# Performance work log

Hardware: AMD Instinct MI355X
Metric: run time of the kernel (lower is better)

## Reference

```python
import jax, jax.numpy as jnp
import numpy as np

INPUT_SIZE = 512
N_THETA = 608  # backcast 512 + forecast 96
N_EXPERTS = 8
TOP_K = 2
LN_EPS = 1e-5


def setup_inputs() -> dict:
    key = jax.random.key(0)
    ks = jax.random.split(key, 5)
    B = 8192
    s = 0.02
    return {
        "insample_y": jax.random.normal(ks[0], (B, INPUT_SIZE), dtype=jnp.float32),
        "ln_gamma": jnp.ones((INPUT_SIZE,), dtype=jnp.float32),
        "ln_beta": jnp.zeros((INPUT_SIZE,), dtype=jnp.float32),
        "Wg": jax.random.normal(ks[1], (INPUT_SIZE, N_EXPERTS), dtype=jnp.float32) * s,
        "W0": jax.random.normal(ks[2], (N_EXPERTS, INPUT_SIZE, 512), dtype=jnp.float32) * s,
        "Wmid": jax.random.normal(ks[3], (3, N_EXPERTS, 512, 512), dtype=jnp.float32) * s,
        "Wout": jax.random.normal(ks[4], (N_EXPERTS, 512, N_THETA), dtype=jnp.float32) * s,
    }


def _layer_norm(x, gamma, beta):
    mu = jnp.mean(x, axis=-1, keepdims=True)
    var = jnp.mean(jnp.square(x - mu), axis=-1, keepdims=True)
    return (x - mu) * jax.lax.rsqrt(var + LN_EPS) * gamma + beta


def reference(insample_y, ln_gamma, ln_beta, Wg, W0, Wmid, Wout):
    x = insample_y  # [B, input_size]
    # Gate: LayerNorm -> Linear(no bias) -> top-k -> softmax over selected logits
    gate_logits = _layer_norm(x, ln_gamma, ln_beta) @ Wg            # [B, E]
    top_vals, top_idx = jax.lax.top_k(gate_logits, TOP_K)           # [B, k]
    gate_w = jax.nn.softmax(top_vals, axis=-1)                      # [B, k]

    # Experts (bias-free MLPs), evaluated densely for all experts
    z = jnp.einsum('bi,eih->beh', x, W0)                            # first linear, no activation
    for l in range(Wmid.shape[0]):
        z = jax.nn.relu(jnp.einsum('beh,eho->beo', z, Wmid[l]))
    theta_all = jnp.einsum('beh,eht->bet', z, Wout)                 # [B, E, n_theta]

    # Combine top-k expert outputs with gate weights
    theta_sel = jnp.take_along_axis(theta_all, top_idx[:, :, None], axis=1)  # [B, k, n_theta]
    theta = jnp.einsum('bk,bkt->bt', gate_w, theta_sel)             # [B, n_theta]

    # Identity basis: split theta into backcast / forecast
    backcast = theta[:, :INPUT_SIZE]
    forecast = theta[:, INPUT_SIZE:]
    return backcast, forecast
```

## Files before the change

kernel.cpp:

```cpp
#include <hip/hip_runtime.h>
#include <hip/hip_bf16.h>
#include <stdint.h>


#define B_ROWS 8192
#define I_DIM  512
#define H_DIM  512
#define E_NUM  8
#define T_DIM  608
#define T_PAD  640
#define CAP    2304
#define TPE    18
#define NT     144
#define NPAD   18432

typedef unsigned short ushort_t;
typedef __attribute__((ext_vector_type(8))) __bf16 bf16x8;
typedef __attribute__((ext_vector_type(8))) unsigned short ushort8;
typedef __attribute__((ext_vector_type(4))) float floatx4;

__device__ __forceinline__ void gload_lds16(const void* g, void* l) {
  __builtin_amdgcn_global_load_lds(
      (const __attribute__((address_space(1))) unsigned int*)g,
      (__attribute__((address_space(3))) unsigned int*)l, 16, 0, 0);
}

__device__ __forceinline__ ushort_t f2bf(float v) {
  __hip_bfloat16 h = __float2bfloat16(v);
  return __builtin_bit_cast(unsigned short, h);
}

__global__ __launch_bounds__(256) void gate_cast_k(
    const float* __restrict__ x, const float* __restrict__ gamma,
    const float* __restrict__ beta, const float* __restrict__ Wg,
    ushort_t* __restrict__ xb, int2* __restrict__ gidx, float2* __restrict__ gw)
{
  const int row  = (blockIdx.x * blockDim.x + threadIdx.x) >> 6;
  const int lane = threadIdx.x & 63;
  const float* xr = x + (size_t)row * I_DIM + lane * 8;
  float4 a = *(const float4*)(xr);
  float4 b = *(const float4*)(xr + 4);
  float xs[8] = {a.x, a.y, a.z, a.w, b.x, b.y, b.z, b.w};

  float s = 0.f;
#pragma unroll
  for (int j = 0; j < 8; ++j) s += xs[j];
#pragma unroll
  for (int off = 32; off; off >>= 1) s += __shfl_xor(s, off);
  const float mu = s * (1.0f / I_DIM);

  float vs = 0.f;
#pragma unroll
  for (int j = 0; j < 8; ++j) { float d = xs[j] - mu; vs += d * d; }
#pragma unroll
  for (int off = 32; off; off >>= 1) vs += __shfl_xor(vs, off);
  const float rstd = rsqrtf(vs * (1.0f / I_DIM) + 1e-5f);

  float lg[8] = {0.f, 0.f, 0.f, 0.f, 0.f, 0.f, 0.f, 0.f};
  const float* gmr = gamma + lane * 8;
  const float* btr = beta + lane * 8;
#pragma unroll
  for (int j = 0; j < 8; ++j) {
    const float y = (xs[j] - mu) * rstd * gmr[j] + btr[j];
    const float* wr = Wg + (size_t)(lane * 8 + j) * E_NUM;
#pragma unroll
    for (int e = 0; e < 8; ++e) lg[e] += y * wr[e];
  }
#pragma unroll
  for (int e = 0; e < 8; ++e)
#pragma unroll
    for (int off = 32; off; off >>= 1) lg[e] += __shfl_xor(lg[e], off);

  ushort8 o;
#pragma unroll
  for (int j = 0; j < 8; ++j) o[j] = f2bf(xs[j]);
  *(ushort8*)(xb + (size_t)row * I_DIM + lane * 8) = o;

  if (lane == 0) {
    int i0 = 0; float b0 = lg[0];
#pragma unroll
    for (int e = 1; e < 8; ++e) if (lg[e] > b0) { b0 = lg[e]; i0 = e; }
    int i1 = -1; float b1 = -3.4e38f;
#pragma unroll
    for (int e = 0; e < 8; ++e) if (e != i0 && lg[e] > b1) { b1 = lg[e]; i1 = e; }
    const float w0 = 1.0f / (1.0f + __expf(b1 - b0));
    gidx[row] = make_int2(i0, i1);
    gw[row] = make_float2(w0, 1.0f - w0);
  }
}

__global__ __launch_bounds__(256) void assign_k(
    const int2* __restrict__ gidx, const float2* __restrict__ gw,
    int* __restrict__ rowmap, float* __restrict__ wmap,
    int* __restrict__ cursor)
{
  __shared__ int lcnt[E_NUM];
  __shared__ int lbase[E_NUM];
  const int tid = threadIdx.x;
  const int row = blockIdx.x * 256 + tid;
  if (tid < E_NUM) lcnt[tid] = 0;
  __syncthreads();
  const int2 g = gidx[row];
  const float2 w = gw[row];
  const int r0 = atomicAdd(&lcnt[g.x], 1);
  const int r1 = atomicAdd(&lcnt[g.y], 1);
  __syncthreads();
  if (tid < E_NUM) lbase[tid] = atomicAdd(&cursor[tid], lcnt[tid]);
  __syncthreads();
  const int p0 = g.x * CAP + lbase[g.x] + r0;
  rowmap[p0] = row; wmap[p0] = w.x;
  const int p1 = g.y * CAP + lbase[g.y] + r1;
  rowmap[p1] = row; wmap[p1] = w.y;
}

__global__ __launch_bounds__(256) void transpose_cast_k(
    const float* __restrict__ src, ushort_t* __restrict__ dst,
    int R, int C, size_t srcBStr, size_t dstBStr)
{
  __shared__ float tile[32][33];
  src += (size_t)blockIdx.z * srcBStr;
  dst += (size_t)blockIdx.z * dstBStr;
  const int c0 = blockIdx.x * 32, r0 = blockIdx.y * 32;
  const int tx = threadIdx.x, ty = threadIdx.y;
#pragma unroll
  for (int i = 0; i < 4; ++i)
    tile[ty + i * 8][tx] = src[(size_t)(r0 + ty + i * 8) * C + c0 + tx];
  __syncthreads();
#pragma unroll
  for (int i = 0; i < 4; ++i) {
    const int c = c0 + ty + i * 8;
    if (c < C) dst[(size_t)c * R + r0 + tx] = f2bf(tile[tx][ty + i * 8]);
  }
}

template <bool GATHER, bool RELU, bool FINAL>
__global__ __launch_bounds__(256) void gemm_k(
    const ushort_t* __restrict__ A,
    const ushort_t* __restrict__ B,
    size_t bEStr,
    const int* __restrict__ rowmap, const float* __restrict__ wmap,
    const int* __restrict__ cursor,
    ushort_t* __restrict__ Z,
    float* __restrict__ out)
{
  constexpr int K = 512;
  __shared__ ushort_t lA[128 * 32];
  __shared__ ushort_t lB[128 * 32];
  __shared__ float wrow[128];
  __shared__ int rrow[128];

  const int t = blockIdx.x;
  const int e = t / TPE;
  if ((t - e * TPE) * 128 >= cursor[e]) return;
  const int zr0 = t * 128;
  const int bn0 = blockIdx.y * 128;

  const int tid = threadIdx.x, wid = tid >> 6, lane = tid & 63;
  const int sr = wid * 16 + (lane >> 2);
  const int sc = (lane & 3) * 8;

  const ushort_t* Bb = B + (size_t)e * bEStr + (size_t)bn0 * K;
  const ushort_t* gb = Bb + (size_t)sr * K + sc;
  const ushort_t *ga0, *ga1;
  if (GATHER) {
    ga0 = A + (size_t)rowmap[zr0 + sr] * K + sc;
    ga1 = A + (size_t)rowmap[zr0 + sr + 64] * K + sc;
  } else {
    ga0 = A + (size_t)(zr0 + sr) * K + sc;
    ga1 = ga0 + (size_t)64 * K;
  }
  ushort_t* la = lA + wid * 512;
  ushort_t* lb = lB + wid * 512;

  floatx4 acc[4][4] = {};
  const int wm = (wid >> 1) * 64, wn = (wid & 1) * 64;
  const int fr = lane & 15, q = lane >> 4;

  for (int k0 = 0; k0 < K; k0 += 32) {
    gload_lds16(ga0 + k0, la);
    gload_lds16(ga1 + k0, la + 64 * 32);
    gload_lds16(gb + k0, lb);
    gload_lds16(gb + (size_t)64 * K + k0, lb + 64 * 32);
    __syncthreads();

    bf16x8 af[4], bfr[4];
#pragma unroll
    for (int mi = 0; mi < 4; ++mi)
      af[mi] = *(const bf16x8*)(lA + (wm + mi * 16 + fr) * 32 + q * 8);
#pragma unroll
    for (int ni = 0; ni < 4; ++ni)
      bfr[ni] = *(const bf16x8*)(lB + (wn + ni * 16 + fr) * 32 + q * 8);
#pragma unroll
    for (int mi = 0; mi < 4; ++mi)
#pragma unroll
      for (int ni = 0; ni < 4; ++ni)
        acc[mi][ni] = __builtin_amdgcn_mfma_f32_16x16x32_bf16(
            af[mi], bfr[ni], acc[mi][ni], 0, 0, 0);
    __syncthreads();
  }

  if (!FINAL) {
    ushort_t* Zb = Z + (size_t)zr0 * H_DIM + bn0;
#pragma unroll
    for (int mi = 0; mi < 4; ++mi)
#pragma unroll
      for (int r = 0; r < 4; ++r) {
        const int row = wm + mi * 16 + q * 4 + r;
        ushort_t* zr = Zb + (size_t)row * H_DIM + wn + fr;
#pragma unroll
        for (int ni = 0; ni < 4; ++ni) {
          float v = acc[mi][ni][r];
          if (RELU) v = fmaxf(v, 0.0f);
          zr[ni * 16] = f2bf(v);
        }
      }
  } else {
    if (tid < 128) {
      wrow[tid] = wmap[zr0 + tid];
      rrow[tid] = rowmap[zr0 + tid];
    }
    __syncthreads();
#pragma unroll
    for (int mi = 0; mi < 4; ++mi)
#pragma unroll
      for (int r = 0; r < 4; ++r) {
        const int row = wm + mi * 16 + q * 4 + r;
        const float w = wrow[row];
        if (w != 0.0f) {
          const size_t orig = rrow[row];
#pragma unroll
          for (int ni = 0; ni < 4; ++ni) {
            const int col = bn0 + wn + ni * 16 + fr;
            if (col < T_DIM) {
              const float v = acc[mi][ni][r] * w;
              float* dst = (col < I_DIM)
                  ? out + orig * I_DIM + col
                  : out + (size_t)B_ROWS * I_DIM + orig * (T_DIM - I_DIM) +
                        (col - I_DIM);
              atomicAdd(dst, v);
            }
          }
        }
      }
  }
}

extern "C" void kernel_launch(void* const* d_in, const int* in_sizes, int n_in,
                              void* d_out, int out_size, void* d_ws,
                              size_t ws_size, hipStream_t stream) {
  const float* x     = (const float*)d_in[0];
  const float* gamma = (const float*)d_in[1];
  const float* beta  = (const float*)d_in[2];
  const float* Wg    = (const float*)d_in[3];
  const float* W0    = (const float*)d_in[4];
  const float* Wmid  = (const float*)d_in[5];
  const float* Wout  = (const float*)d_in[6];
  float* out = (float*)d_out;

  char* ws = (char*)d_ws;
  size_t off = 0;
  auto alloc = [&](size_t bytes) -> char* {
    char* p = ws + off;
    off += (bytes + 255) & ~(size_t)255;
    return p;
  };

  const size_t SQ = (size_t)H_DIM * H_DIM;
  ushort_t* xb    = (ushort_t*)alloc((size_t)B_ROWS * I_DIM * 2);
  ushort_t* W0t   = (ushort_t*)alloc((size_t)E_NUM * SQ * 2);
  ushort_t* Wmidt = (ushort_t*)alloc((size_t)3 * E_NUM * SQ * 2);
  ushort_t* Woutt = (ushort_t*)alloc((size_t)E_NUM * T_PAD * H_DIM * 2);
  int2*   gidx  = (int2*)alloc((size_t)B_ROWS * sizeof(int2));
  float2* gwv   = (float2*)alloc((size_t)B_ROWS * sizeof(float2));
  int*   rmap   = (int*)alloc(NPAD * sizeof(int));
  float* wmap   = (float*)alloc(NPAD * sizeof(float));
  int*   cursor = (int*)alloc(E_NUM * sizeof(int));
  ushort_t* z0 = (ushort_t*)alloc((size_t)NPAD * H_DIM * 2);
  ushort_t* z1 = (ushort_t*)alloc((size_t)NPAD * H_DIM * 2);

  hipMemsetAsync(d_out, 0, (size_t)out_size * sizeof(float), stream);
  hipMemsetAsync(rmap, 0, NPAD * sizeof(int), stream);
  hipMemsetAsync(wmap, 0, NPAD * sizeof(float), stream);
  hipMemsetAsync(cursor, 0, E_NUM * sizeof(int), stream);

  gate_cast_k<<<dim3(B_ROWS / 4), 256, 0, stream>>>(x, gamma, beta, Wg, xb,
                                                    gidx, gwv);
  transpose_cast_k<<<dim3(16, 16, 8), dim3(32, 8), 0, stream>>>(
      W0, W0t, 512, 512, SQ, SQ);
  transpose_cast_k<<<dim3(16, 16, 24), dim3(32, 8), 0, stream>>>(
      Wmid, Wmidt, 512, 512, SQ, SQ);
  transpose_cast_k<<<dim3(19, 16, 8), dim3(32, 8), 0, stream>>>(
      Wout, Woutt, 512, 608, (size_t)512 * 608, (size_t)T_PAD * 512);
  assign_k<<<dim3(B_ROWS / 256), 256, 0, stream>>>(gidx, gwv, rmap, wmap,
                                                   cursor);

  const dim3 gmid(NT, H_DIM / 128);
  const dim3 gfin(NT, T_PAD / 128);
  gemm_k<true, false, false><<<gmid, 256, 0, stream>>>(
      xb, W0t, SQ, rmap, wmap, cursor, z0, nullptr);
  gemm_k<false, true, false><<<gmid, 256, 0, stream>>>(
      z0, Wmidt + 0 * E_NUM * SQ, SQ, rmap, wmap, cursor, z1, nullptr);
  gemm_k<false, true, false><<<gmid, 256, 0, stream>>>(
      z1, Wmidt + 1 * E_NUM * SQ, SQ, rmap, wmap, cursor, z0, nullptr);
  gemm_k<false, true, false><<<gmid, 256, 0, stream>>>(
      z0, Wmidt + 2 * E_NUM * SQ, SQ, rmap, wmap, cursor, z1, nullptr);
  gemm_k<false, false, true><<<gfin, 256, 0, stream>>>(
      z1, Woutt, (size_t)T_PAD * H_DIM, rmap, wmap, cursor, nullptr, out);
}
```

Before: 257.4 us.

## Double-buffer GEMM LDS tiles with register prefetch to overlap loads and MFMA

Replaces the direct global-to-LDS loads with register prefetch into uint4 values followed by stores into two alternating LDS buffers. The next K-slice is fetched while MFMAs run on the current buffer, which removes one barrier per iteration and hides global latency. In exchange it doubles LDS use for the tiles, adds register pressure, and adds an extra register-to-LDS store path.

```diff
diff --git a/kernel.cpp b/kernel.cpp
--- a/kernel.cpp
+++ b/kernel.cpp
@@ -18,12 +18,6 @@
 typedef __attribute__((ext_vector_type(8))) __bf16 bf16x8;
 typedef __attribute__((ext_vector_type(8))) unsigned short ushort8;
 typedef __attribute__((ext_vector_type(4))) float floatx4;
-
-__device__ __forceinline__ void gload_lds16(const void* g, void* l) {
-  __builtin_amdgcn_global_load_lds(
-      (const __attribute__((address_space(1))) unsigned int*)g,
-      (__attribute__((address_space(3))) unsigned int*)l, 16, 0, 0);
-}
 
 __device__ __forceinline__ ushort_t f2bf(float v) {
   __hip_bfloat16 h = __float2bfloat16(v);
@@ -144,8 +138,8 @@
     float* __restrict__ out)
 {
   constexpr int K = 512;
-  __shared__ ushort_t lA[128 * 32];
-  __shared__ ushort_t lB[128 * 32];
+  __shared__ ushort_t lA[2][128 * 32];
+  __shared__ ushort_t lB[2][128 * 32];
   __shared__ float wrow[128];
   __shared__ int rrow[128];
 
@@ -160,7 +154,8 @@
   const int sc = (lane & 3) * 8;
 
   const ushort_t* Bb = B + (size_t)e * bEStr + (size_t)bn0 * K;
-  const ushort_t* gb = Bb + (size_t)sr * K + sc;
+  const ushort_t* gb0 = Bb + (size_t)sr * K + sc;
+  const ushort_t* gb1 = gb0 + (size_t)64 * K;
   const ushort_t *ga0, *ga1;
   if (GATHER) {
     ga0 = A + (size_t)rowmap[zr0 + sr] * K + sc;
@@ -169,34 +164,58 @@
     ga0 = A + (size_t)(zr0 + sr) * K + sc;
     ga1 = ga0 + (size_t)64 * K;
   }
-  ushort_t* la = lA + wid * 512;
-  ushort_t* lb = lB + wid * 512;
+  const int lw = wid * 512 + lane * 8;
 
   floatx4 acc[4][4] = {};
   const int wm = (wid >> 1) * 64, wn = (wid & 1) * 64;
   const int fr = lane & 15, q = lane >> 4;
 
-  for (int k0 = 0; k0 < K; k0 += 32) {
-    gload_lds16(ga0 + k0, la);
-    gload_lds16(ga1 + k0, la + 64 * 32);
-    gload_lds16(gb + k0, lb);
-    gload_lds16(gb + (size_t)64 * K + k0, lb + 64 * 32);
-    __syncthreads();
-
+  uint4 rA0, rA1, rB0, rB1;
+  auto prefetch = [&](int k) {
+    rA0 = *(const uint4*)(ga0 + k);
+    rA1 = *(const uint4*)(ga1 + k);
+    rB0 = *(const uint4*)(gb0 + k);
+    rB1 = *(const uint4*)(gb1 + k);
+  };
+  auto stage = [&](int buf) {
+    *(uint4*)(&lA[buf][lw])        = rA0;
+    *(uint4*)(&lA[buf][2048 + lw]) = rA1;
+    *(uint4*)(&lB[buf][lw])        = rB0;
+    *(uint4*)(&lB[buf][2048 + lw]) = rB1;
+  };
+  auto compute = [&](int buf) {
     bf16x8 af[4], bfr[4];
 #pragma unroll
     for (int mi = 0; mi < 4; ++mi)
-      af[mi] = *(const bf16x8*)(lA + (wm + mi * 16 + fr) * 32 + q * 8);
+      af[mi] = *(const bf16x8*)(&lA[buf][(wm + mi * 16 + fr) * 32 + q * 8]);
 #pragma unroll
     for (int ni = 0; ni < 4; ++ni)
-      bfr[ni] = *(const bf16x8*)(lB + (wn + ni * 16 + fr) * 32 + q * 8);
+      bfr[ni] = *(const bf16x8*)(&lB[buf][(wn + ni * 16 + fr) * 32 + q * 8]);
 #pragma unroll
     for (int mi = 0; mi < 4; ++mi)
 #pragma unroll
       for (int ni = 0; ni < 4; ++ni)
         acc[mi][ni] = __builtin_amdgcn_mfma_f32_16x16x32_bf16(
             af[mi], bfr[ni], acc[mi][ni], 0, 0, 0);
+  };
+
+  prefetch(0);
+  stage(0);
+
+#pragma unroll 1
+  for (int k0 = 0; k0 < K; k0 += 64) {
     __syncthreads();
+    prefetch(k0 + 32);
+    compute(0);
+    stage(1);
+    __syncthreads();
+    if (k0 < K - 64) {
+      prefetch(k0 + 64);
+      compute(1);
+      stage(0);
+    } else {
+      compute(1);
+    }
   }
 
   if (!FINAL) {
```

Result: slower. 293.3 us (+13.9%).

## Software-pipeline GEMM K-loop with register prefetch and double-buffered LDS

Applied to the files above, without the earlier changes.

Replaces direct global-to-LDS loads with a register-staged pipeline: each thread keeps three K-chunks of A/B in flight in registers and writes the next chunk into a second LDS buffer while MFMAs run on the current one. This leaves one barrier per K-step instead of two and is meant to hide global load latency behind compute. It also moves the FINAL-path gate weight and row map loads before the main loop, which removes one barrier from the epilogue. The cost is higher register pressure from 12 uint4 staging registers plus the accumulators, which may lower occupancy, and double the LDS footprint.

```diff
diff --git a/kernel.cpp b/kernel.cpp
--- a/kernel.cpp
+++ b/kernel.cpp
@@ -18,12 +18,6 @@
 typedef __attribute__((ext_vector_type(8))) __bf16 bf16x8;
 typedef __attribute__((ext_vector_type(8))) unsigned short ushort8;
 typedef __attribute__((ext_vector_type(4))) float floatx4;
-
-__device__ __forceinline__ void gload_lds16(const void* g, void* l) {
-  __builtin_amdgcn_global_load_lds(
-      (const __attribute__((address_space(1))) unsigned int*)g,
-      (__attribute__((address_space(3))) unsigned int*)l, 16, 0, 0);
-}
 
 __device__ __forceinline__ ushort_t f2bf(float v) {
   __hip_bfloat16 h = __float2bfloat16(v);
@@ -144,8 +138,9 @@
     float* __restrict__ out)
 {
   constexpr int K = 512;
-  __shared__ ushort_t lA[128 * 32];
-  __shared__ ushort_t lB[128 * 32];
+  constexpr int NCH = K / 32;
+  __shared__ ushort_t lA[2][128 * 32];
+  __shared__ ushort_t lB[2][128 * 32];
   __shared__ float wrow[128];
   __shared__ int rrow[128];
 
@@ -160,7 +155,8 @@
   const int sc = (lane & 3) * 8;
 
   const ushort_t* Bb = B + (size_t)e * bEStr + (size_t)bn0 * K;
-  const ushort_t* gb = Bb + (size_t)sr * K + sc;
+  const ushort_t* gb0 = Bb + (size_t)sr * K + sc;
+  const ushort_t* gb1 = gb0 + (size_t)64 * K;
   const ushort_t *ga0, *ga1;
   if (GATHER) {
     ga0 = A + (size_t)rowmap[zr0 + sr] * K + sc;
@@ -169,33 +165,62 @@
     ga0 = A + (size_t)(zr0 + sr) * K + sc;
     ga1 = ga0 + (size_t)64 * K;
   }
-  ushort_t* la = lA + wid * 512;
-  ushort_t* lb = lB + wid * 512;
+
+  if (FINAL) {
+    if (tid < 128) {
+      wrow[tid] = wmap[zr0 + tid];
+      rrow[tid] = rowmap[zr0 + tid];
+    }
+  }
+
+  const int lw = wid * 512 + lane * 8;
 
   floatx4 acc[4][4] = {};
   const int wm = (wid >> 1) * 64, wn = (wid & 1) * 64;
   const int fr = lane & 15, q = lane >> 4;
 
-  for (int k0 = 0; k0 < K; k0 += 32) {
-    gload_lds16(ga0 + k0, la);
-    gload_lds16(ga1 + k0, la + 64 * 32);
-    gload_lds16(gb + k0, lb);
-    gload_lds16(gb + (size_t)64 * K + k0, lb + 64 * 32);
-    __syncthreads();
-
+  uint4 sA0[3], sA1[3], sB0[3], sB1[3];
+  auto ld = [&](int c) {
+    const int s = c % 3;
+    const int k = c * 32;
+    sA0[s] = *(const uint4*)(ga0 + k);
+    sA1[s] = *(const uint4*)(ga1 + k);
+    sB0[s] = *(const uint4*)(gb0 + k);
+    sB1[s] = *(const uint4*)(gb1 + k);
+  };
+  auto stage = [&](int c) {
+    const int s = c % 3, b = c & 1;
+    *(uint4*)(&lA[b][lw])        = sA0[s];
+    *(uint4*)(&lA[b][2048 + lw]) = sA1[s];
+    *(uint4*)(&lB[b][lw])        = sB0[s];
+    *(uint4*)(&lB[b][2048 + lw]) = sB1[s];
+  };
+  auto compute = [&](int c) {
+    const int b = c & 1;
     bf16x8 af[4], bfr[4];
 #pragma unroll
     for (int mi = 0; mi < 4; ++mi)
-      af[mi] = *(const bf16x8*)(lA + (wm + mi * 16 + fr) * 32 + q * 8);
+      af[mi] = *(const bf16x8*)(&lA[b][(wm + mi * 16 + fr) * 32 + q * 8]);
 #pragma unroll
     for (int ni = 0; ni < 4; ++ni)
-      bfr[ni] = *(const bf16x8*)(lB + (wn + ni * 16 + fr) * 32 + q * 8);
+      bfr[ni] = *(const bf16x8*)(&lB[b][(wn + ni * 16 + fr) * 32 + q * 8]);
 #pragma unroll
     for (int mi = 0; mi < 4; ++mi)
 #pragma unroll
       for (int ni = 0; ni < 4; ++ni)
         acc[mi][ni] = __builtin_amdgcn_mfma_f32_16x16x32_bf16(
             af[mi], bfr[ni], acc[mi][ni], 0, 0, 0);
+  };
+
+  ld(0); ld(1); ld(2);
+  stage(0);
+  __syncthreads();
+
+#pragma unroll
+  for (int c = 0; c < NCH; ++c) {
+    if (c + 3 < NCH) ld(c + 3);
+    compute(c);
+    if (c + 1 < NCH) stage(c + 1);
     __syncthreads();
   }
 
@@ -215,11 +240,6 @@
         }
       }
   } else {
-    if (tid < 128) {
-      wrow[tid] = wmap[zr0 + tid];
-      rrow[tid] = rowmap[zr0 + tid];
-    }
-    __syncthreads();
 #pragma unroll
     for (int mi = 0; mi < 4; ++mi)
 #pragma unroll
```

Measured after the change: 476.2 us. 85.0% more time.
